# Optimization experiments

Measured on AMD Instinct MI355X. Metric: run time of the kernel, lower is better.

## Reference

```python
import jax, jax.numpy as jnp
import numpy as np

D_MODEL, N_HEADS = 1024, 16
D_H = D_MODEL // N_HEADS          # 64
D_HR = D_H // 2                   # 32 (decoupled RoPE dim)
D_LATENT = 256
THETA = 10000.0


def rope(x, theta=THETA):
    # x: (..., S, d) with d even; rotate interleaved pairs.
    S, d = x.shape[-2], x.shape[-1]
    inv = theta ** (-jnp.arange(0, d, 2, dtype=jnp.float32) / d)      # (d/2,)
    ang = jnp.arange(S, dtype=jnp.float32)[:, None] * inv             # (S, d/2)
    cos, sin = jnp.cos(ang), jnp.sin(ang)
    x1, x2 = x[..., 0::2], x[..., 1::2]
    r1 = x1 * cos - x2 * sin
    r2 = x1 * sin + x2 * cos
    return jnp.stack([r1, r2], axis=-1).reshape(x.shape)


def setup_inputs() -> dict:
    key = jax.random.key(0)
    ks = jax.random.split(key, 9)
    s = lambda fan_in: 1.0 / np.sqrt(fan_in)
    return {
        "x": jax.random.normal(ks[0], (4, 2048, D_MODEL), jnp.float32),
        "W_DQ": jax.random.normal(ks[1], (D_MODEL, D_LATENT), jnp.float32) * s(D_MODEL),
        "W_UQ": jax.random.normal(ks[2], (D_LATENT, N_HEADS * D_H), jnp.float32) * s(D_LATENT),
        "W_QR": jax.random.normal(ks[3], (D_LATENT, N_HEADS * D_HR), jnp.float32) * s(D_LATENT),
        "W_DKV": jax.random.normal(ks[4], (D_MODEL, D_LATENT), jnp.float32) * s(D_MODEL),
        "W_UK": jax.random.normal(ks[5], (D_LATENT, N_HEADS * D_H), jnp.float32) * s(D_LATENT),
        "W_UV": jax.random.normal(ks[6], (D_LATENT, N_HEADS * D_H), jnp.float32) * s(D_LATENT),
        "W_KR": jax.random.normal(ks[7], (D_MODEL, D_HR), jnp.float32) * s(D_MODEL),
        "W_O": jax.random.normal(ks[8], (N_HEADS * D_H, D_MODEL), jnp.float32) * s(N_HEADS * D_H),
    }


def reference(x, W_DQ, W_UQ, W_QR, W_DKV, W_UK, W_UV, W_KR, W_O):
    B, S, _ = x.shape
    d_qk = D_H + D_HR

    # --- query path: low-rank latent + decoupled RoPE ---
    c_q = x @ W_DQ                                                   # (B,S,L)
    Qc = (c_q @ W_UQ).reshape(B, S, N_HEADS, D_H).transpose(0, 2, 1, 3)   # (B,H,S,dh)
    Qr = (c_q @ W_QR).reshape(B, S, N_HEADS, D_HR).transpose(0, 2, 1, 3)  # (B,H,S,dhr)
    Qr = rope(Qr)

    # --- key/value path: shared latent, shared rotary key ---
    c_kv = x @ W_DKV                                                 # (B,S,L)
    Kc = (c_kv @ W_UK).reshape(B, S, N_HEADS, D_H).transpose(0, 2, 1, 3)  # (B,H,S,dh)
    Kr = rope((x @ W_KR)[:, None, :, :])                             # (B,1,S,dhr)
    Kr = jnp.broadcast_to(Kr, (B, N_HEADS, S, D_HR))
    V = (c_kv @ W_UV).reshape(B, S, N_HEADS, D_H).transpose(0, 2, 1, 3)   # (B,H,S,dh)

    Q = jnp.concatenate([Qc, Qr], axis=-1)                           # (B,H,S,d_qk)
    K = jnp.concatenate([Kc, Kr], axis=-1)

    scores = jnp.einsum('bhqd,bhkd->bhqk', Q, K)
    scores = jnp.clip(scores, -80.0, 80.0)
    causal = jnp.tril(jnp.ones((S, S), dtype=bool))
    scores = jnp.where(causal, scores, -jnp.inf)
    weights = jax.nn.softmax(scores / jnp.sqrt(jnp.float32(d_qk)), axis=-1)
    attn = jnp.einsum('bhqk,bhkd->bhqd', weights, V)                 # (B,H,S,dh)
    attn = attn.transpose(0, 2, 1, 3).reshape(B, S, N_HEADS * D_H)
    return attn @ W_O
```

## Files before the change

### kernel.cpp

```cpp
#include <hip/hip_runtime.h>
#include <hip/hip_bf16.h>


typedef __attribute__((ext_vector_type(8))) __bf16 bf16x8;
typedef __attribute__((ext_vector_type(4))) float f32x4;
typedef __attribute__((ext_vector_type(16))) float f32x16;
typedef __attribute__((ext_vector_type(4))) unsigned short us4;

#define DEV static __device__ __forceinline__

DEV unsigned short f2b(float f) {
  union { __hip_bfloat16 h; unsigned short u; } v;
  v.h = __float2bfloat16(f);
  return v.u;
}
DEV float b2f(unsigned short u) {
  union { unsigned short u; __hip_bfloat16 h; } v;
  v.u = u;
  return __bfloat162float(v.h);
}
DEV unsigned int f2b2(float lo, float hi) {
  union { __hip_bfloat162 h2; unsigned int u; } v;
  float2 t; t.x = lo; t.y = hi;
  v.h2 = __float22bfloat162_rn(t);
  return v.u;
}
DEV f32x4 mfma16(bf16x8 a, bf16x8 b, f32x4 c) {
  return __builtin_amdgcn_mfma_f32_16x16x32_bf16(a, b, c, 0, 0, 0);
}
DEV f32x16 mfma32(bf16x8 a, bf16x8 b, f32x16 c) {
  return __builtin_amdgcn_mfma_f32_32x32x16_bf16(a, b, c, 0, 0, 0);
}
DEV void load_lds16(const void* g, void* lds) {
  __builtin_amdgcn_global_load_lds((__attribute__((address_space(1))) void*)g,
                                   (__attribute__((address_space(3))) void*)lds,
                                   16, 0, 0);
}

#define KSC2f 0.14724444690f
#define CLIPf 11.7795557220f

__global__ __launch_bounds__(256) void convert_x(const float* __restrict__ x,
                                                 unsigned short* __restrict__ xb) {
  long i = (long)(blockIdx.x * 256 + threadIdx.x) * 4;
  float4 v = *(const float4*)(x + i);
  us4 o = { f2b(v.x), f2b(v.y), f2b(v.z), f2b(v.w) };
  *(us4*)(xb + i) = o;
}

struct TWArgs { const float* W[8]; unsigned short* T[8]; };
__global__ __launch_bounds__(256) void transpose_w_all(TWArgs a) {
  int bid = blockIdx.x;
  int g;
  if      (bid < 256)  g = 0;
  else if (bid < 512)  g = 1;
  else if (bid < 544)  g = 2;
  else if (bid < 800)  g = 3;
  else if (bid < 928)  g = 4;
  else if (bid < 1184) g = 5;
  else if (bid < 1440) g = 6;
  else                 g = 7;
  const int starts[8] = {0, 256, 512, 544, 800, 928, 1184, 1440};
  int local = bid - starts[g];
  int K = (g >= 3 && g <= 6) ? 256 : 1024;
  int N = (g < 2) ? 256 : (g == 2 ? 32 : (g == 4 ? 512 : 1024));
  int tilesX = N >> 5;
  int n0 = (local % tilesX) * 32, k0 = (local / tilesX) * 32;
  const float* W = a.W[g];
  unsigned short* WT = a.T[g];
  float sc = (g == 3 || g == 4) ? KSC2f : 1.0f;
  __shared__ float tile[32][33];
  int tx = threadIdx.x & 31, ty = threadIdx.x >> 5;
#pragma unroll
  for (int i = 0; i < 32; i += 8)
    tile[ty + i][tx] = W[(size_t)(k0 + ty + i) * N + n0 + tx];
  __syncthreads();
#pragma unroll
  for (int i = 0; i < 32; i += 8)
    WT[(size_t)(n0 + ty + i) * K + k0 + tx] = f2b(tile[tx][ty + i] * sc);
}

__global__ __launch_bounds__(256) void rope_qk(unsigned short* __restrict__ C2,
                                               const unsigned short* __restrict__ C1,
                                               unsigned short* __restrict__ Krr) {
  if (blockIdx.x < 8192) {
    int idx = blockIdx.x * 256 + threadIdx.x;
    int i = idx & 15, h = (idx >> 4) & 15, s = (idx >> 8) & 2047, b = idx >> 19;
    long base = (long)(b * 2048 + s) * 1536 + 1024 + h * 32 + 2 * i;
    float x1 = b2f(C2[base]), x2 = b2f(C2[base + 1]);
    float inv = exp2f(-(float)i * 0.8304820237686285f);
    float ang = (float)s * inv;
    float c = cosf(ang), sn = sinf(ang);
    C2[base]     = f2b(x1 * c - x2 * sn);
    C2[base + 1] = f2b(x1 * sn + x2 * c);
  } else {
    int idx = (blockIdx.x - 8192) * 256 + threadIdx.x;
    int i = idx & 15, s = (idx >> 4) & 2047, b = idx >> 15;
    long src = (long)(b * 2048 + s) * 544 + 512 + 2 * i;
    float x1 = b2f(C1[src]), x2 = b2f(C1[src + 1]);
    float inv = exp2f(-(float)i * 0.8304820237686285f);
    float ang = (float)s * inv;
    float c = cosf(ang), sn = sinf(ang);
    long dst = (long)(b * 2048 + s) * 32 + 2 * i;
    Krr[dst]     = f2b(x1 * c - x2 * sn);
    Krr[dst + 1] = f2b(x1 * sn + x2 * c);
  }
}

template <bool OUT_BF16>
__global__ __launch_bounds__(256) void gemm_bt(const unsigned short* __restrict__ A, int lda,
                                               const unsigned short* __restrict__ Bt, int ldb,
                                               void* __restrict__ Cv, int ldc, int N, int K) {
  __shared__ __align__(16) unsigned short As[128 * 32];
  __shared__ __align__(16) unsigned short Bs[128 * 32];
  const int t = threadIdx.x;
  const int w = t >> 6, lane = t & 63, ln = lane & 15, quad = lane >> 4;
  const int wr = w >> 1, wc = w & 1;
  const int bm0 = blockIdx.x * 128, bn0 = blockIdx.y * 128;
  const int srow = t >> 2;
  const int scol = (t & 3) * 8;
  f32x4 zero = {0.f, 0.f, 0.f, 0.f};
  f32x4 acc[4][4];
#pragma unroll
  for (int i = 0; i < 4; ++i)
#pragma unroll
    for (int j = 0; j < 4; ++j) acc[i][j] = zero;

  for (int k0 = 0; k0 < K; k0 += 32) {
#pragma unroll
    for (int r = 0; r < 2; ++r) {
      int arow = bm0 + r * 64 + srow;
      load_lds16(A + (long)arow * lda + k0 + scol, (char*)As + r * 4096 + w * 1024);
      int brow = bn0 + r * 64 + srow;
      if (brow > N - 1) brow = N - 1;
      load_lds16(Bt + (long)brow * ldb + k0 + scol, (char*)Bs + r * 4096 + w * 1024);
    }
    __syncthreads();
    bf16x8 af[4], bf[4];
#pragma unroll
    for (int i = 0; i < 4; ++i)
      af[i] = *(const bf16x8*)(As + (wr * 64 + i * 16 + ln) * 32 + quad * 8);
#pragma unroll
    for (int j = 0; j < 4; ++j)
      bf[j] = *(const bf16x8*)(Bs + (wc * 64 + j * 16 + ln) * 32 + quad * 8);
#pragma unroll
    for (int i = 0; i < 4; ++i)
#pragma unroll
      for (int j = 0; j < 4; ++j) acc[i][j] = mfma16(af[i], bf[j], acc[i][j]);
    __syncthreads();
  }
#pragma unroll
  for (int i = 0; i < 4; ++i)
#pragma unroll
    for (int j = 0; j < 4; ++j)
#pragma unroll
      for (int r = 0; r < 4; ++r) {
        int row = bm0 + wr * 64 + i * 16 + quad * 4 + r;
        int col = bn0 + wc * 64 + j * 16 + ln;
        if (col < N) {
          if (OUT_BF16)
            ((unsigned short*)Cv)[(long)row * ldc + col] = f2b(acc[i][j][r]);
          else
            ((float*)Cv)[(long)row * ldc + col] = acc[i][j][r];
        }
      }
}

__global__ __launch_bounds__(256) void gemm_bt_vt(const unsigned short* __restrict__ A, int lda,
                                                  const unsigned short* __restrict__ Bt, int ldb,
                                                  unsigned short* __restrict__ Vt, int K) {
  __shared__ __align__(16) unsigned short As[128 * 32];
  __shared__ __align__(16) unsigned short Bs[128 * 32];
  const int t = threadIdx.x;
  const int w = t >> 6, lane = t & 63, ln = lane & 15, quad = lane >> 4;
  const int wr = w >> 1, wc = w & 1;
  const int bm0 = blockIdx.x * 128, bn0 = blockIdx.y * 128;
  const int srow = t >> 2, scol = (t & 3) * 8;
  f32x4 zero = {0.f, 0.f, 0.f, 0.f};
  f32x4 acc[4][4];
#pragma unroll
  for (int i = 0; i < 4; ++i)
#pragma unroll
    for (int j = 0; j < 4; ++j) acc[i][j] = zero;

  for (int k0 = 0; k0 < K; k0 += 32) {
#pragma unroll
    for (int r = 0; r < 2; ++r) {
      load_lds16(A + (long)(bm0 + r * 64 + srow) * lda + k0 + scol, (char*)As + r * 4096 + w * 1024);
      load_lds16(Bt + (long)(bn0 + r * 64 + srow) * ldb + k0 + scol, (char*)Bs + r * 4096 + w * 1024);
    }
    __syncthreads();
    bf16x8 af[4], bf[4];
#pragma unroll
    for (int i = 0; i < 4; ++i)
      af[i] = *(const bf16x8*)(As + (wr * 64 + i * 16 + ln) * 32 + quad * 8);
#pragma unroll
    for (int j = 0; j < 4; ++j)
      bf[j] = *(const bf16x8*)(Bs + (wc * 64 + j * 16 + ln) * 32 + quad * 8);
#pragma unroll
    for (int i = 0; i < 4; ++i)
#pragma unroll
      for (int j = 0; j < 4; ++j) acc[i][j] = mfma16(af[i], bf[j], acc[i][j]);
    __syncthreads();
  }
#pragma unroll
  for (int i = 0; i < 4; ++i)
#pragma unroll
    for (int j = 0; j < 4; ++j) {
      int col = bn0 + wc * 64 + j * 16 + ln;
      int row0 = bm0 + wr * 64 + i * 16 + quad * 4;
      int b = row0 >> 11, sl = row0 & 2047;
      us4 pk = { f2b(acc[i][j][0]), f2b(acc[i][j][1]), f2b(acc[i][j][2]), f2b(acc[i][j][3]) };
      *(us4*)(Vt + ((size_t)(b * 16) * 64 + col) * 2048 + sl) = pk;
    }
}

__global__ __launch_bounds__(256, 3) void flash_attn(const unsigned short* __restrict__ C2,
                                                     const unsigned short* __restrict__ C3,
                                                     const unsigned short* __restrict__ Krr,
                                                     const unsigned short* __restrict__ Vt,
                                                     unsigned short* __restrict__ Oa) {
  __shared__ __align__(16) unsigned short Ks[2][4096];
  __shared__ __align__(16) unsigned short Vs[2][4096];

  const int tid = threadIdx.x;
  const int w = tid >> 6, lane = tid & 63;
  const int l31 = lane & 31, h = lane >> 5;
  const int bh = blockIdx.x, b = bh >> 4, head = bh & 15;
  const int bS = b * 2048;
  const int qi = 15 - (int)blockIdx.y;
  const int qb = qi * 128 + w * 32;
  const int nkt = 2 * qi + 2;
  const int q = qb + l31;
  const int pr = (l31 & ~12) | ((l31 & 4) << 1) | ((l31 & 8) >> 1);

  const unsigned short* qp = C2 + (size_t)(bS + q) * 1536;
  bf16x8 qf[6];
#pragma unroll
  for (int c = 0; c < 4; ++c)
    qf[c] = *(const bf16x8*)(qp + head * 64 + c * 16 + h * 8);
#pragma unroll
  for (int c = 4; c < 6; ++c)
    qf[c] = *(const bf16x8*)(qp + 1024 + head * 32 + (c - 4) * 16 + h * 8);

  union { unsigned short u[8]; bf16x8 v; } onesu;
#pragma unroll
  for (int i = 0; i < 8; ++i) onesu.u[i] = 0x3F80;
  const bf16x8 ones = onesu.v;

  f32x16 o0 = {}, o1 = {}, osum = {};

  auto stage = [&](int buf, int key0) {
#pragma unroll
    for (int t = w; t < 8; t += 4) {
      int ci = t * 64 + lane;
      int r = ci >> 3, sl = ci & 7;
      int srcc = sl ^ (r & 7) ^ (r >> 3);
      int srck = (r & ~12) | ((r & 4) << 1) | ((r & 8) >> 1);
      load_lds16(C3 + (size_t)(bS + key0 + srck) * 1024 + head * 64 + srcc * 8,
                 &Ks[buf][t * 512]);
    }
#pragma unroll
    for (int t = w; t < 8; t += 4) {
      int ci = t * 64 + lane;
      int r = ci >> 3, sl = ci & 7;
      int srcc = sl ^ (r & 7) ^ (r >> 3);
      load_lds16(Vt + (size_t)((size_t)bh * 64 + r) * 2048 + key0 + srcc * 8,
                 &Vs[buf][t * 512]);
    }
  };

  stage(0, 0);
  for (int kt = 0; kt < nkt; ++kt) {
    __syncthreads();
    const int c0 = kt * 64;
    const bool live = (c0 <= qb + 31);
    bf16x8 kr[4];
    if (live) {
#pragma unroll
      for (int m = 0; m < 2; ++m)
#pragma unroll
        for (int c = 0; c < 2; ++c)
          kr[m * 2 + c] = *(const bf16x8*)(Krr + (size_t)(bS + c0 + m * 32 + pr) * 32 +
                                           c * 16 + h * 8);
    }
    if (kt + 1 < nkt) stage((kt + 1) & 1, c0 + 64);
    if (!live) continue;

    const unsigned short* Kp = Ks[kt & 1];
    const unsigned short* Vp = Vs[kt & 1];

#pragma unroll
    for (int m = 0; m < 2; ++m) {
      if (c0 + m * 32 > qb + 31) continue;
      const int r = m * 32 + l31;
      f32x16 s = {};
#pragma unroll
      for (int c = 0; c < 4; ++c) {
        int slot = (2 * c + h) ^ (r & 7) ^ (r >> 3);
        bf16x8 kf = *(const bf16x8*)(Kp + r * 64 + slot * 8);
        s = mfma32(kf, qf[c], s);
      }
      s = mfma32(kr[m * 2 + 0], qf[4], s);
      s = mfma32(kr[m * 2 + 1], qf[5], s);

      const bool nm = (c0 + m * 32 + 31) > qb;
      float ev[16];
#pragma unroll
      for (int p = 0; p < 16; ++p) {
        float z = __builtin_amdgcn_fmed3f(s[p], -CLIPf, CLIPf);
        if (nm) {
          int key = c0 + m * 32 + (p & 3) + 4 * ((p >> 2) & 1) + 8 * h + 16 * (p >> 3);
          if (key > q) z = -1e30f;
        }
        ev[p] = exp2f(z);
      }
      bf16x8 pf[2];
#pragma unroll
      for (int t = 0; t < 2; ++t) {
        union { unsigned int u[4]; bf16x8 v; } pk;
#pragma unroll
        for (int j = 0; j < 4; ++j)
          pk.u[j] = f2b2(ev[t * 8 + 2 * j], ev[t * 8 + 2 * j + 1]);
        pf[t] = pk.v;
      }
#pragma unroll
      for (int t = 0; t < 2; ++t) {
        int tk = m * 2 + t;
        osum = mfma32(pf[t], ones, osum);
#pragma unroll
        for (int n = 0; n < 2; ++n) {
          int rr = n * 32 + l31;
          int slot = (2 * tk + h) ^ (rr & 7) ^ (rr >> 3);
          bf16x8 vf = *(const bf16x8*)(Vp + rr * 64 + slot * 8);
          if (n == 0) o0 = mfma32(pf[t], vf, o0);
          else        o1 = mfma32(pf[t], vf, o1);
        }
      }
    }
  }

#pragma unroll
  for (int p = 0; p < 16; ++p) {
    int qrow = (p & 3) + 8 * (p >> 2) + 4 * h;
    float rl = 1.0f / osum[p];
    size_t base = (size_t)(bS + qb + qrow) * 1024 + head * 64;
    Oa[base + l31]      = f2b(o0[p] * rl);
    Oa[base + 32 + l31] = f2b(o1[p] * rl);
  }
}

extern "C" void kernel_launch(void* const* d_in, const int* in_sizes, int n_in,
                              void* d_out, int out_size, void* d_ws, size_t ws_size,
                              hipStream_t stream) {
  (void)in_sizes; (void)n_in; (void)out_size; (void)ws_size;
  const float* x     = (const float*)d_in[0];
  const float* W_DQ  = (const float*)d_in[1];
  const float* W_UQ  = (const float*)d_in[2];
  const float* W_QR  = (const float*)d_in[3];
  const float* W_DKV = (const float*)d_in[4];
  const float* W_UK  = (const float*)d_in[5];
  const float* W_UV  = (const float*)d_in[6];
  const float* W_KR  = (const float*)d_in[7];
  const float* W_O   = (const float*)d_in[8];

  char* p = (char*)d_ws;
  unsigned short* xb  = (unsigned short*)p; p += (size_t)8192 * 1024 * 2;
  unsigned short* WT1 = (unsigned short*)p; p += (size_t)544 * 1024 * 2;
  unsigned short* WT2 = (unsigned short*)p; p += (size_t)1536 * 256 * 2;
  unsigned short* WT3 = (unsigned short*)p; p += (size_t)2048 * 256 * 2;
  unsigned short* WT4 = (unsigned short*)p; p += (size_t)1024 * 1024 * 2;
  unsigned short* C1  = (unsigned short*)p; p += (size_t)8192 * 544 * 2;
  unsigned short* C2  = (unsigned short*)p; p += (size_t)8192 * 1536 * 2;
  unsigned short* C3  = (unsigned short*)p; p += (size_t)8192 * 1024 * 2;
  unsigned short* Krr = (unsigned short*)p; p += (size_t)8192 * 32 * 2;
  unsigned short* Vt  = (unsigned short*)p; p += (size_t)64 * 64 * 2048 * 2;
  unsigned short* Oa  = (unsigned short*)p; p += (size_t)8192 * 1024 * 2;

  convert_x<<<8192, 256, 0, stream>>>(x, xb);

  TWArgs tw;
  tw.W[0] = W_DQ;  tw.T[0] = WT1;
  tw.W[1] = W_DKV; tw.T[1] = WT1 + 256 * 1024;
  tw.W[2] = W_KR;  tw.T[2] = WT1 + 512 * 1024;
  tw.W[3] = W_UQ;  tw.T[3] = WT2;
  tw.W[4] = W_QR;  tw.T[4] = WT2 + 1024 * 256;
  tw.W[5] = W_UK;  tw.T[5] = WT3;
  tw.W[6] = W_UV;  tw.T[6] = WT3 + 1024 * 256;
  tw.W[7] = W_O;   tw.T[7] = WT4;
  transpose_w_all<<<2464, 256, 0, stream>>>(tw);

  gemm_bt<true><<<dim3(64, 5),  256, 0, stream>>>(xb, 1024, WT1, 1024, C1, 544, 544, 1024);
  gemm_bt<true><<<dim3(64, 12), 256, 0, stream>>>(C1, 544, WT2, 256, C2, 1536, 1536, 256);
  gemm_bt<true><<<dim3(64, 8),  256, 0, stream>>>(C1 + 256, 544, WT3, 256, C3, 1024, 1024, 256);
  gemm_bt_vt<<<dim3(64, 8),     256, 0, stream>>>(C1 + 256, 544, WT3 + 1024 * 256, 256, Vt, 256);
  rope_qk<<<8704, 256, 0, stream>>>(C2, C1, Krr);
  flash_attn<<<dim3(64, 16), 256, 0, stream>>>(C2, C3, Krr, Vt, Oa);
  gemm_bt<false><<<dim3(64, 8), 256, 0, stream>>>(Oa, 1024, WT4, 1024, d_out, 1024, 1024, 1024);
}
```

Baseline: 284.0 us.

## Merge K/V up-projection launches, reorder query tiles, prefetch rotary keys

The separate Kc and V up-projection GEMMs become a single launch with 16 column-blocks, where blocks with y>=8 write the transposed V layout. In flash attention, query-tile order is permuted to balance causal work across the grid, and the rotary-key fragments for the next tile are loaded after the current tile's compute instead of before it. This is meant to cut a kernel launch, improve load balance, and hide Krr global-load latency, at the cost of keeping the kr registers live across iterations.

```diff
diff --git a/kernel.cpp b/kernel.cpp
--- a/kernel.cpp
+++ b/kernel.cpp
@@ -166,15 +166,18 @@
       }
 }
 
-__global__ __launch_bounds__(256) void gemm_bt_vt(const unsigned short* __restrict__ A, int lda,
-                                                  const unsigned short* __restrict__ Bt, int ldb,
-                                                  unsigned short* __restrict__ Vt, int K) {
+__global__ __launch_bounds__(256) void gemm_kv(const unsigned short* __restrict__ A, int lda,
+                                               const unsigned short* __restrict__ Bt0,
+                                               unsigned short* __restrict__ C3,
+                                               unsigned short* __restrict__ Vt) {
   __shared__ __align__(16) unsigned short As[128 * 32];
   __shared__ __align__(16) unsigned short Bs[128 * 32];
   const int t = threadIdx.x;
   const int w = t >> 6, lane = t & 63, ln = lane & 15, quad = lane >> 4;
   const int wr = w >> 1, wc = w & 1;
-  const int bm0 = blockIdx.x * 128, bn0 = blockIdx.y * 128;
+  const bool isV = blockIdx.y >= 8;
+  const unsigned short* Bt = Bt0 + (isV ? (size_t)1024 * 256 : 0);
+  const int bm0 = blockIdx.x * 128, bn0 = (blockIdx.y & 7) * 128;
   const int srow = t >> 2, scol = (t & 3) * 8;
   f32x4 zero = {0.f, 0.f, 0.f, 0.f};
   f32x4 acc[4][4];
@@ -183,11 +186,11 @@
 #pragma unroll
     for (int j = 0; j < 4; ++j) acc[i][j] = zero;
 
-  for (int k0 = 0; k0 < K; k0 += 32) {
+  for (int k0 = 0; k0 < 256; k0 += 32) {
 #pragma unroll
     for (int r = 0; r < 2; ++r) {
       load_lds16(A + (long)(bm0 + r * 64 + srow) * lda + k0 + scol, (char*)As + r * 4096 + w * 1024);
-      load_lds16(Bt + (long)(bn0 + r * 64 + srow) * ldb + k0 + scol, (char*)Bs + r * 4096 + w * 1024);
+      load_lds16(Bt + (long)(bn0 + r * 64 + srow) * 256 + k0 + scol, (char*)Bs + r * 4096 + w * 1024);
     }
     __syncthreads();
     bf16x8 af[4], bf[4];
@@ -203,16 +206,29 @@
       for (int j = 0; j < 4; ++j) acc[i][j] = mfma16(af[i], bf[j], acc[i][j]);
     __syncthreads();
   }
-#pragma unroll
-  for (int i = 0; i < 4; ++i)
-#pragma unroll
-    for (int j = 0; j < 4; ++j) {
-      int col = bn0 + wc * 64 + j * 16 + ln;
-      int row0 = bm0 + wr * 64 + i * 16 + quad * 4;
-      int b = row0 >> 11, sl = row0 & 2047;
-      us4 pk = { f2b(acc[i][j][0]), f2b(acc[i][j][1]), f2b(acc[i][j][2]), f2b(acc[i][j][3]) };
-      *(us4*)(Vt + ((size_t)(b * 16) * 64 + col) * 2048 + sl) = pk;
-    }
+  if (!isV) {
+#pragma unroll
+    for (int i = 0; i < 4; ++i)
+#pragma unroll
+      for (int j = 0; j < 4; ++j)
+#pragma unroll
+        for (int r = 0; r < 4; ++r) {
+          int row = bm0 + wr * 64 + i * 16 + quad * 4 + r;
+          int col = bn0 + wc * 64 + j * 16 + ln;
+          C3[(long)row * 1024 + col] = f2b(acc[i][j][r]);
+        }
+  } else {
+#pragma unroll
+    for (int i = 0; i < 4; ++i)
+#pragma unroll
+      for (int j = 0; j < 4; ++j) {
+        int col = bn0 + wc * 64 + j * 16 + ln;
+        int row0 = bm0 + wr * 64 + i * 16 + quad * 4;
+        int b = row0 >> 11, sl = row0 & 2047;
+        us4 pk = { f2b(acc[i][j][0]), f2b(acc[i][j][1]), f2b(acc[i][j][2]), f2b(acc[i][j][3]) };
+        *(us4*)(Vt + ((size_t)(b * 16) * 64 + col) * 2048 + sl) = pk;
+      }
+  }
 }
 
 __global__ __launch_bounds__(256, 3) void flash_attn(const unsigned short* __restrict__ C2,
@@ -228,7 +244,8 @@
   const int l31 = lane & 31, h = lane >> 5;
   const int bh = blockIdx.x, b = bh >> 4, head = bh & 15;
   const int bS = b * 2048;
-  const int qi = 15 - (int)blockIdx.y;
+  const int QPERM[16] = {15, 14, 13, 12, 8, 9, 10, 11, 4, 5, 6, 7, 3, 2, 1, 0};
+  const int qi = QPERM[blockIdx.y];
   const int qb = qi * 128 + w * 32;
   const int nkt = 2 * qi + 2;
   const int q = qb + l31;
@@ -270,74 +287,78 @@
     }
   };
 
+  auto load_kr = [&](bf16x8* kr, int c0) {
+#pragma unroll
+    for (int m = 0; m < 2; ++m)
+#pragma unroll
+      for (int c = 0; c < 2; ++c)
+        kr[m * 2 + c] = *(const bf16x8*)(Krr + (size_t)(bS + c0 + m * 32 + pr) * 32 +
+                                         c * 16 + h * 8);
+  };
+
+  bf16x8 kr[4];
+  load_kr(kr, 0);
   stage(0, 0);
   for (int kt = 0; kt < nkt; ++kt) {
     __syncthreads();
     const int c0 = kt * 64;
     const bool live = (c0 <= qb + 31);
-    bf16x8 kr[4];
+    if (kt + 1 < nkt) stage((kt + 1) & 1, c0 + 64);
+
     if (live) {
-#pragma unroll
-      for (int m = 0; m < 2; ++m)
-#pragma unroll
-        for (int c = 0; c < 2; ++c)
-          kr[m * 2 + c] = *(const bf16x8*)(Krr + (size_t)(bS + c0 + m * 32 + pr) * 32 +
-                                           c * 16 + h * 8);
-    }
-    if (kt + 1 < nkt) stage((kt + 1) & 1, c0 + 64);
-    if (!live) continue;
-
-    const unsigned short* Kp = Ks[kt & 1];
-    const unsigned short* Vp = Vs[kt & 1];
-
-#pragma unroll
-    for (int m = 0; m < 2; ++m) {
-      if (c0 + m * 32 > qb + 31) continue;
-      const int r = m * 32 + l31;
-      f32x16 s = {};
-#pragma unroll
-      for (int c = 0; c < 4; ++c) {
-        int slot = (2 * c + h) ^ (r & 7) ^ (r >> 3);
-        bf16x8 kf = *(const bf16x8*)(Kp + r * 64 + slot * 8);
-        s = mfma32(kf, qf[c], s);
-      }
-      s = mfma32(kr[m * 2 + 0], qf[4], s);
-      s = mfma32(kr[m * 2 + 1], qf[5], s);
-
-      const bool nm = (c0 + m * 32 + 31) > qb;
-      float ev[16];
-#pragma unroll
-      for (int p = 0; p < 16; ++p) {
-        float z = __builtin_amdgcn_fmed3f(s[p], -CLIPf, CLIPf);
-        if (nm) {
-          int key = c0 + m * 32 + (p & 3) + 4 * ((p >> 2) & 1) + 8 * h + 16 * (p >> 3);
-          if (key > q) z = -1e30f;
-        }
-        ev[p] = exp2f(z);
-      }
-      bf16x8 pf[2];
-#pragma unroll
-      for (int t = 0; t < 2; ++t) {
-        union { unsigned int u[4]; bf16x8 v; } pk;
-#pragma unroll
-        for (int j = 0; j < 4; ++j)
-          pk.u[j] = f2b2(ev[t * 8 + 2 * j], ev[t * 8 + 2 * j + 1]);
-        pf[t] = pk.v;
-      }
-#pragma unroll
-      for (int t = 0; t < 2; ++t) {
-        int tk = m * 2 + t;
-        osum = mfma32(pf[t], ones, osum);
-#pragma unroll
-        for (int n = 0; n < 2; ++n) {
-          int rr = n * 32 + l31;
-          int slot = (2 * tk + h) ^ (rr & 7) ^ (rr >> 3);
-          bf16x8 vf = *(const bf16x8*)(Vp + rr * 64 + slot * 8);
-          if (n == 0) o0 = mfma32(pf[t], vf, o0);
-          else        o1 = mfma32(pf[t], vf, o1);
+      const unsigned short* Kp = Ks[kt & 1];
+      const unsigned short* Vp = Vs[kt & 1];
+
+#pragma unroll
+      for (int m = 0; m < 2; ++m) {
+        if (c0 + m * 32 > qb + 31) continue;
+        const int r = m * 32 + l31;
+        f32x16 s = {};
+#pragma unroll
+        for (int c = 0; c < 4; ++c) {
+          int slot = (2 * c + h) ^ (r & 7) ^ (r >> 3);
+          bf16x8 kf = *(const bf16x8*)(Kp + r * 64 + slot * 8);
+          s = mfma32(kf, qf[c], s);
+        }
+        s = mfma32(kr[m * 2 + 0], qf[4], s);
+        s = mfma32(kr[m * 2 + 1], qf[5], s);
+
+        const bool nm = (c0 + m * 32 + 31) > qb;
+        float ev[16];
+#pragma unroll
+        for (int p = 0; p < 16; ++p) {
+          float z = __builtin_amdgcn_fmed3f(s[p], -CLIPf, CLIPf);
+          if (nm) {
+            int key = c0 + m * 32 + (p & 3) + 4 * ((p >> 2) & 1) + 8 * h + 16 * (p >> 3);
+            if (key > q) z = -1e30f;
+          }
+          ev[p] = exp2f(z);
+        }
+        bf16x8 pf[2];
+#pragma unroll
+        for (int t = 0; t < 2; ++t) {
+          union { unsigned int u[4]; bf16x8 v; } pk;
+#pragma unroll
+          for (int j = 0; j < 4; ++j)
+            pk.u[j] = f2b2(ev[t * 8 + 2 * j], ev[t * 8 + 2 * j + 1]);
+          pf[t] = pk.v;
+        }
+#pragma unroll
+        for (int t = 0; t < 2; ++t) {
+          int tk = m * 2 + t;
+          osum = mfma32(pf[t], ones, osum);
+#pragma unroll
+          for (int n = 0; n < 2; ++n) {
+            int rr = n * 32 + l31;
+            int slot = (2 * tk + h) ^ (rr & 7) ^ (rr >> 3);
+            bf16x8 vf = *(const bf16x8*)(Vp + rr * 64 + slot * 8);
+            if (n == 0) o0 = mfma32(pf[t], vf, o0);
+            else        o1 = mfma32(pf[t], vf, o1);
+          }
         }
       }
     }
+    if (kt + 1 < nkt && (c0 + 64 <= qb + 31)) load_kr(kr, c0 + 64);
   }
 
 #pragma unroll
@@ -392,8 +413,7 @@
 
   gemm_bt<true><<<dim3(64, 5),  256, 0, stream>>>(xb, 1024, WT1, 1024, C1, 544, 544, 1024);
   gemm_bt<true><<<dim3(64, 12), 256, 0, stream>>>(C1, 544, WT2, 256, C2, 1536, 1536, 256);
-  gemm_bt<true><<<dim3(64, 8),  256, 0, stream>>>(C1 + 256, 544, WT3, 256, C3, 1024, 1024, 256);
-  gemm_bt_vt<<<dim3(64, 8),     256, 0, stream>>>(C1 + 256, 544, WT3 + 1024 * 256, 256, Vt, 256);
+  gemm_kv<<<dim3(64, 16),       256, 0, stream>>>(C1 + 256, 544, WT3, C3, Vt);
   rope_qk<<<8704, 256, 0, stream>>>(C2, C1, Krr);
   flash_attn<<<dim3(64, 16), 256, 0, stream>>>(C2, C3, Krr, Vt, Oa);
   gemm_bt<false><<<dim3(64, 8), 256, 0, stream>>>(Oa, 1024, WT4, 1024, d_out, 1024, 1024, 1024);
```

Result: no change. 282.2 us (-0.6%).
